# Performance work log

Measured on AMD Instinct MI355X. Metric: run time of the kernel, lower is better.

Reference implementation:

```python
import jax, jax.numpy as jnp
import numpy as np

N = 100000
E = 1600000
D = 128


def setup_inputs() -> dict:
    key = jax.random.key(0)
    k1, k2, k3 = jax.random.split(key, 3)
    indices = jax.random.randint(k1, (2, E), 0, N, dtype=jnp.int32)
    values = jax.random.uniform(k2, (E,), dtype=jnp.float32)
    b = jax.random.normal(k3, (N, D), dtype=jnp.float32)
    return {"values": values, "b": b, "indices": indices, "n": N}


def reference(values, b, indices, n):
    # out = sparse_coo(indices, values, (n, n)) @ b
    # out[i] = sum_{e: row_e == i} values[e] * b[col_e]
    row, col = indices[0], indices[1]
    return jax.ops.segment_sum(values[:, None] * b[col], row, num_segments=n)
```

## Files before the change

### kernel.cpp

```cpp
#include <hip/hip_runtime.h>


#define D_DIM    128
#define RPB      64
#define COLBITS  17
#define COLMASK  ((1 << COLBITS) - 1)
#define NCMAX    512
#define NBMAX    1600
#define CAP      2048
#define NXCD     8

__device__ __forceinline__ unsigned bfr_rne(float f) {
    unsigned u = __float_as_uint(f);
    return (u + 0x7fffu + ((u >> 16) & 1u)) >> 16;
}
__device__ __forceinline__ float bf_lo(unsigned u) { return __uint_as_float(u << 16); }
__device__ __forceinline__ float bf_hi(unsigned u) { return __uint_as_float(u & 0xffff0000u); }

__device__ __forceinline__ int xcd_remap(int bid, int n) {
    int q = n / NXCD, r = n % NXCD;
    int xcd = bid % NXCD, slot = bid / NXCD;
    int base = (xcd < r) ? xcd * (q + 1) : r * (q + 1) + (xcd - r) * q;
    return base + slot;
}

__global__ __launch_bounds__(1024) void k01_fused(
    const int* __restrict__ idx, const float4* __restrict__ b4,
    uint4* __restrict__ bb4, unsigned short* __restrict__ cnt16,
    int E, int NBUX, int CH, int n8) {
    __shared__ int hist[NBMAX];
    int tid = threadIdx.x, c = blockIdx.x;
    int base = c * CH;
    int cnt  = min(CH, E - base);
    for (int i = tid; i < NBUX; i += 1024) hist[i] = 0;
    __syncthreads();
    for (int i = tid; i < cnt; i += 1024)
        atomicAdd(&hist[idx[base + i] >> 6], 1);
    __syncthreads();
    for (int i = tid; i < NBUX; i += 1024)
        cnt16[(size_t)c * NBUX + i] = (unsigned short)hist[i];

    int gstride = gridDim.x * 1024;
    for (int i = blockIdx.x * 1024 + tid; i < n8; i += gstride) {
        float4 a = b4[2 * i];
        float4 d = b4[2 * i + 1];
        uint4 o;
        o.x = bfr_rne(a.x) | (bfr_rne(a.y) << 16);
        o.y = bfr_rne(a.z) | (bfr_rne(a.w) << 16);
        o.z = bfr_rne(d.x) | (bfr_rne(d.y) << 16);
        o.w = bfr_rne(d.z) | (bfr_rne(d.w) << 16);
        bb4[i] = o;
    }
}

__global__ __launch_bounds__(256) void k2a_lofs(
    unsigned short* __restrict__ cnt16, int* __restrict__ total,
    int NCHUNK, int NBUX) {
    int k    = blockIdx.x * 4 + (threadIdx.x >> 6);
    int lane = threadIdx.x & 63;
    if (k >= NBUX) return;
    int PC = (NCHUNK + 63) >> 6;
    int c0 = lane * PC;
    int vals[8];
    int sum = 0;
#pragma unroll
    for (int j = 0; j < 8; ++j) {
        int c = c0 + j;
        vals[j] = (j < PC && c < NCHUNK) ? (int)cnt16[(size_t)c * NBUX + k] : 0;
        sum += vals[j];
    }
    int v = sum;
#pragma unroll
    for (int d = 1; d < 64; d <<= 1) {
        int t = __shfl_up(v, d, 64);
        if (lane >= d) v += t;
    }
    int run = v - sum;
#pragma unroll
    for (int j = 0; j < 8; ++j) {
        int c = c0 + j;
        if (j < PC && c < NCHUNK) {
            cnt16[(size_t)c * NBUX + k] = (unsigned short)run;
            run += vals[j];
        }
    }
    if (lane == 63) total[k] = run;
}

__global__ void k2b_scan(const int* __restrict__ total, int* __restrict__ boff, int n) {
    __shared__ int s[256];
    int t = threadIdx.x;
    int loc[8]; int tot = 0;
#pragma unroll
    for (int j = 0; j < 8; ++j) { int i = t * 8 + j; loc[j] = (i < n) ? total[i] : 0; tot += loc[j]; }
    s[t] = tot; __syncthreads();
    for (int ofs = 1; ofs < 256; ofs <<= 1) {
        int v = (t >= ofs) ? s[t - ofs] : 0; __syncthreads();
        s[t] += v; __syncthreads();
    }
    int run = s[t] - tot;
#pragma unroll
    for (int j = 0; j < 8; ++j) { int i = t * 8 + j; if (i < n) boff[i] = run; run += loc[j]; }
    if (t == 255) boff[n] = s[255];
}

__global__ __launch_bounds__(1024) void k3_scatter(
    const int* __restrict__ idx, const float* __restrict__ values,
    const unsigned short* __restrict__ lofs, const int* __restrict__ boff,
    int2* __restrict__ cv, int E, int NBUX, int CH, int NCHUNK) {
    __shared__ int cur[NBMAX];
    int tid = threadIdx.x;
    int c   = xcd_remap(blockIdx.x, NCHUNK);
    int base = c * CH;
    int cnt  = min(CH, E - base);
    for (int i = tid; i < NBUX; i += 1024)
        cur[i] = boff[i] + (int)lofs[(size_t)c * NBUX + i];
    __syncthreads();
    for (int i = tid; i < cnt; i += 1024) {
        int   row = idx[base + i];
        int   col = idx[E + base + i];
        float v   = values[base + i];
        int pos = atomicAdd(&cur[row >> 6], 1);
        cv[pos] = make_int2(((row & (RPB - 1)) << COLBITS) | col, __float_as_int(v));
    }
}

__global__ __launch_bounds__(256, 8) void k4_reg_bf16(
    const unsigned short* __restrict__ bb, const int2* __restrict__ cv,
    const int* __restrict__ boff, float* __restrict__ out, int N) {
    __shared__ int2 sorted[CAP];
    __shared__ int  rcnt[RPB], roff[RPB], rcur[RPB];

    int tid  = threadIdx.x;
    int lane = tid & 15;
    int grp  = tid >> 4;
    int k    = blockIdx.x;
    int s    = boff[k];
    int cnt  = min(boff[k + 1] - s, CAP);

    if (tid < RPB) rcnt[tid] = 0;

    int2 rec[8];
#pragma unroll
    for (int j = 0; j < 8; ++j) {
        int i = tid + j * 256;
        rec[j] = (i < cnt) ? cv[s + i] : make_int2(0, 0);
    }
    __syncthreads();

#pragma unroll
    for (int j = 0; j < 8; ++j) {
        int i = tid + j * 256;
        if (i < cnt) atomicAdd(&rcnt[rec[j].x >> COLBITS], 1);
    }
    __syncthreads();

    if (tid < 64) {
        int cval = rcnt[tid];
        int v = cval;
#pragma unroll
        for (int d = 1; d < 64; d <<= 1) {
            int t = __shfl_up(v, d, 64);
            if (tid >= d) v += t;
        }
        roff[tid] = v - cval;
        rcur[tid] = v - cval;
    }
    __syncthreads();

#pragma unroll
    for (int j = 0; j < 8; ++j) {
        int i = tid + j * 256;
        if (i < cnt) {
            int pos = atomicAdd(&rcur[rec[j].x >> COLBITS], 1);
            sorted[pos] = rec[j];
        }
    }
    __syncthreads();

    float acc[4][8];
#pragma unroll
    for (int r = 0; r < 4; ++r)
#pragma unroll
        for (int j = 0; j < 8; ++j) acc[r][j] = 0.f;

    const unsigned short* bl = bb + (lane << 3);

#pragma unroll
    for (int r = 0; r < 4; ++r) {
        int lr = (grp << 2) | r;
        int i  = roff[lr];
        int re = rcur[lr];
        for (; i + 1 < re; i += 2) {
            int2 p0 = sorted[i];
            int2 p1 = sorted[i + 1];
            float v0 = __int_as_float(p0.y);
            float v1 = __int_as_float(p1.y);
            const uint4 w0 = *reinterpret_cast<const uint4*>(bl + ((size_t)(p0.x & COLMASK) << 7));
            const uint4 w1 = *reinterpret_cast<const uint4*>(bl + ((size_t)(p1.x & COLMASK) << 7));
            acc[r][0] += v0 * bf_lo(w0.x); acc[r][1] += v0 * bf_hi(w0.x);
            acc[r][2] += v0 * bf_lo(w0.y); acc[r][3] += v0 * bf_hi(w0.y);
            acc[r][4] += v0 * bf_lo(w0.z); acc[r][5] += v0 * bf_hi(w0.z);
            acc[r][6] += v0 * bf_lo(w0.w); acc[r][7] += v0 * bf_hi(w0.w);
            acc[r][0] += v1 * bf_lo(w1.x); acc[r][1] += v1 * bf_hi(w1.x);
            acc[r][2] += v1 * bf_lo(w1.y); acc[r][3] += v1 * bf_hi(w1.y);
            acc[r][4] += v1 * bf_lo(w1.z); acc[r][5] += v1 * bf_hi(w1.z);
            acc[r][6] += v1 * bf_lo(w1.w); acc[r][7] += v1 * bf_hi(w1.w);
        }
        if (i < re) {
            int2 p0 = sorted[i];
            float v0 = __int_as_float(p0.y);
            const uint4 w0 = *reinterpret_cast<const uint4*>(bl + ((size_t)(p0.x & COLMASK) << 7));
            acc[r][0] += v0 * bf_lo(w0.x); acc[r][1] += v0 * bf_hi(w0.x);
            acc[r][2] += v0 * bf_lo(w0.y); acc[r][3] += v0 * bf_hi(w0.y);
            acc[r][4] += v0 * bf_lo(w0.z); acc[r][5] += v0 * bf_hi(w0.z);
            acc[r][6] += v0 * bf_lo(w0.w); acc[r][7] += v0 * bf_hi(w0.w);
        }
    }

#pragma unroll
    for (int r = 0; r < 4; ++r) {
        int row = (k << 6) + (grp << 2) + r;
        if (row < N) {
            float* po = out + ((size_t)row << 7) + (lane << 3);
            *reinterpret_cast<float4*>(po)     = make_float4(acc[r][0], acc[r][1], acc[r][2], acc[r][3]);
            *reinterpret_cast<float4*>(po + 4) = make_float4(acc[r][4], acc[r][5], acc[r][6], acc[r][7]);
        }
    }
}

__global__ __launch_bounds__(256, 8) void k4_sortgather_f32(
    const float* __restrict__ b, const int2* __restrict__ cv,
    const int* __restrict__ boff, float* __restrict__ out, int N) {
    __shared__ int2 sorted[CAP];
    __shared__ int  rcnt[RPB], roff[RPB], rcur[RPB];
    int tid  = threadIdx.x;
    int lane = tid & 31;
    int grp  = tid >> 5;
    int k    = blockIdx.x;
    int s    = boff[k];
    int cnt  = min(boff[k + 1] - s, CAP);
    if (tid < RPB) rcnt[tid] = 0;
    __syncthreads();
    for (int i = tid; i < cnt; i += 256)
        atomicAdd(&rcnt[cv[s + i].x >> COLBITS], 1);
    __syncthreads();
    if (tid < 64) {
        int cval = rcnt[tid];
        int v = cval;
#pragma unroll
        for (int d = 1; d < 64; d <<= 1) {
            int t = __shfl_up(v, d, 64);
            if (tid >= d) v += t;
        }
        roff[tid] = v - cval;
        rcur[tid] = v - cval;
    }
    __syncthreads();
    for (int i = tid; i < cnt; i += 256) {
        int2 p = cv[s + i];
        int pos = atomicAdd(&rcur[p.x >> COLBITS], 1);
        sorted[pos] = p;
    }
    __syncthreads();
    float4 acc[8];
#pragma unroll
    for (int r = 0; r < 8; ++r) acc[r] = make_float4(0.f, 0.f, 0.f, 0.f);
    const float* bl = b + (lane << 2);
#pragma unroll
    for (int r = 0; r < 8; ++r) {
        int lr = (grp << 3) | r;
        int i  = roff[lr];
        int re = rcur[lr];
        for (; i < re; ++i) {
            int2 p0 = sorted[i];
            float v0 = __int_as_float(p0.y);
            const float4 b0 = *reinterpret_cast<const float4*>(bl + (size_t)(p0.x & COLMASK) * D_DIM);
            acc[r].x += v0 * b0.x; acc[r].y += v0 * b0.y;
            acc[r].z += v0 * b0.z; acc[r].w += v0 * b0.w;
        }
    }
#pragma unroll
    for (int r = 0; r < 8; ++r) {
        int row = (k << 6) + (grp << 3) + r;
        if (row < N)
            *reinterpret_cast<float4*>(out + (size_t)row * D_DIM + (lane << 2)) = acc[r];
    }
}

__global__ void spmm_atomic_scatter(const float* __restrict__ values,
                                    const float* __restrict__ b,
                                    const int* __restrict__ indices,
                                    float* __restrict__ out, int E) {
    long long gid = (long long)blockIdx.x * blockDim.x + threadIdx.x;
    long long total = (long long)E * 32;
    if (gid >= total) return;
    int e = (int)(gid >> 5);
    int c = (int)(gid & 31);
    int row = indices[e];
    int col = indices[E + e];
    float v = values[e];
    const float4 bv = *reinterpret_cast<const float4*>(b + (long long)col * D_DIM + (c << 2));
    float* o = out + (long long)row * D_DIM + (c << 2);
    atomicAdd(o + 0, v * bv.x);
    atomicAdd(o + 1, v * bv.y);
    atomicAdd(o + 2, v * bv.z);
    atomicAdd(o + 3, v * bv.w);
}

extern "C" void kernel_launch(void* const* d_in, const int* in_sizes, int n_in,
                              void* d_out, int out_size, void* d_ws, size_t ws_size,
                              hipStream_t stream) {
    const float* values = (const float*)d_in[0];
    const float* b      = (const float*)d_in[1];
    const int*   idx    = (const int*)d_in[2];
    float*       out    = (float*)d_out;

    const int E    = in_sizes[0];
    const int N    = out_size / D_DIM;
    const int NBUX = (N + RPB - 1) / RPB;

    size_t bb_bytes  = ((size_t)N * D_DIM * sizeof(unsigned short) + 15) & ~(size_t)15;
    size_t int_bytes = (((size_t)(NBUX + 1) + NBUX) * sizeof(int) + 15) & ~(size_t)15;
    size_t cv_bytes  = (size_t)E * sizeof(int2);

    int CH = 4096;
    int NCHUNK = (E + CH - 1) / CH;
    size_t c16_bytes = ((size_t)NCHUNK * NBUX * sizeof(unsigned short) + 15) & ~(size_t)15;
    size_t need1 = bb_bytes + int_bytes + c16_bytes + cv_bytes;
    if (ws_size < need1 || NCHUNK > NCMAX) {
        CH = 8192;
        NCHUNK = (E + CH - 1) / CH;
        c16_bytes = ((size_t)NCHUNK * NBUX * sizeof(unsigned short) + 15) & ~(size_t)15;
        need1 = bb_bytes + int_bytes + c16_bytes + cv_bytes;
    }
    size_t need2 = int_bytes + c16_bytes + cv_bytes;

    bool ok_shape = (NBUX <= NBMAX) && (NCHUNK <= NCMAX) && (N <= (1 << COLBITS));
    if (!ok_shape || ws_size < need2) {
        hipMemsetAsync(d_out, 0, (size_t)out_size * sizeof(float), stream);
        long long total = (long long)E * 32;
        int block = 256;
        long long grid = (total + block - 1) / block;
        spmm_atomic_scatter<<<(int)grid, block, 0, stream>>>(values, b, idx, out, E);
        return;
    }

    bool use_bf16 = (ws_size >= need1);
    char* base = (char*)d_ws;
    unsigned short* bb = (unsigned short*)base;
    if (use_bf16) base += bb_bytes;

    int*            boff  = (int*)base;
    int*            total = boff + (NBUX + 1);
    unsigned short* cnt16 = (unsigned short*)(base + int_bytes);
    int2*           cv    = (int2*)(base + int_bytes + c16_bytes);

    int n8 = use_bf16 ? (N * D_DIM) / 8 : 0;
    k01_fused<<<NCHUNK, 1024, 0, stream>>>(idx, (const float4*)b, (uint4*)bb,
                                           cnt16, E, NBUX, CH, n8);
    k2a_lofs<<<(NBUX + 3) / 4, 256, 0, stream>>>(cnt16, total, NCHUNK, NBUX);
    k2b_scan<<<1, 256, 0, stream>>>(total, boff, NBUX);
    k3_scatter<<<NCHUNK, 1024, 0, stream>>>(idx, values, cnt16, boff, cv, E, NBUX, CH, NCHUNK);
    if (use_bf16)
        k4_reg_bf16<<<NBUX, 256, 0, stream>>>(bb, cv, boff, out, N);
    else
        k4_sortgather_f32<<<NBUX, 256, 0, stream>>>(b, cv, boff, out, N);
}
```

Baseline: 107.7 us.

## Vectorize index loads, add nontemporal hints, merge scan kernels via last-block pattern

Row and column indices and values are now read as 4-wide vectors in the histogram and scatter kernels. Streaming loads and stores of b, the packed records and the output use nontemporal hints. The per-bucket scan and the global scan kernel are merged into one launch: the last block to finish, found through an atomic counter, runs the final scan. This removes one launch and cuts load instruction count, at the cost of a threadfence/atomic handshake and an extra alignment guard.

Result: slower. 135.0 us (+25.3%).

```diff
diff --git a/kernel.cpp b/kernel.cpp
--- a/kernel.cpp
+++ b/kernel.cpp
@@ -10,6 +10,10 @@
 #define CAP      2048
 #define NXCD     8
 
+typedef int   i32x4 __attribute__((ext_vector_type(4)));
+typedef float f32x4 __attribute__((ext_vector_type(4)));
+typedef unsigned int u32x4 __attribute__((ext_vector_type(4)));
+
 __device__ __forceinline__ unsigned bfr_rne(float f) {
     unsigned u = __float_as_uint(f);
     return (u + 0x7fffu + ((u >> 16) & 1u)) >> 16;
@@ -25,16 +29,27 @@
 }
 
 __global__ __launch_bounds__(1024) void k01_fused(
-    const int* __restrict__ idx, const float4* __restrict__ b4,
-    uint4* __restrict__ bb4, unsigned short* __restrict__ cnt16,
-    int E, int NBUX, int CH, int n8) {
+    const int* __restrict__ idx, const u32x4* __restrict__ b4,
+    u32x4* __restrict__ bb4, unsigned short* __restrict__ cnt16,
+    int* __restrict__ done, int E, int NBUX, int CH, int n8) {
     __shared__ int hist[NBMAX];
     int tid = threadIdx.x, c = blockIdx.x;
     int base = c * CH;
     int cnt  = min(CH, E - base);
+    if (c == 0 && tid == 0) *done = 0;
     for (int i = tid; i < NBUX; i += 1024) hist[i] = 0;
     __syncthreads();
-    for (int i = tid; i < cnt; i += 1024)
+
+    int nv4 = cnt >> 2;
+    const i32x4* rows4 = (const i32x4*)(idx + base);
+    for (int i = tid; i < nv4; i += 1024) {
+        i32x4 r = rows4[i];
+        atomicAdd(&hist[r.x >> 6], 1);
+        atomicAdd(&hist[r.y >> 6], 1);
+        atomicAdd(&hist[r.z >> 6], 1);
+        atomicAdd(&hist[r.w >> 6], 1);
+    }
+    for (int i = (nv4 << 2) + tid; i < cnt; i += 1024)
         atomicAdd(&hist[idx[base + i] >> 6], 1);
     __syncthreads();
     for (int i = tid; i < NBUX; i += 1024)
@@ -42,72 +57,84 @@
 
     int gstride = gridDim.x * 1024;
     for (int i = blockIdx.x * 1024 + tid; i < n8; i += gstride) {
-        float4 a = b4[2 * i];
-        float4 d = b4[2 * i + 1];
-        uint4 o;
-        o.x = bfr_rne(a.x) | (bfr_rne(a.y) << 16);
-        o.y = bfr_rne(a.z) | (bfr_rne(a.w) << 16);
-        o.z = bfr_rne(d.x) | (bfr_rne(d.y) << 16);
-        o.w = bfr_rne(d.z) | (bfr_rne(d.w) << 16);
+        u32x4 a = __builtin_nontemporal_load(b4 + 2 * i);
+        u32x4 d = __builtin_nontemporal_load(b4 + 2 * i + 1);
+        u32x4 o;
+        o.x = bfr_rne(__uint_as_float(a.x)) | (bfr_rne(__uint_as_float(a.y)) << 16);
+        o.y = bfr_rne(__uint_as_float(a.z)) | (bfr_rne(__uint_as_float(a.w)) << 16);
+        o.z = bfr_rne(__uint_as_float(d.x)) | (bfr_rne(__uint_as_float(d.y)) << 16);
+        o.w = bfr_rne(__uint_as_float(d.z)) | (bfr_rne(__uint_as_float(d.w)) << 16);
         bb4[i] = o;
     }
 }
 
-__global__ __launch_bounds__(256) void k2a_lofs(
+__global__ __launch_bounds__(256) void k2_merged(
     unsigned short* __restrict__ cnt16, int* __restrict__ total,
-    int NCHUNK, int NBUX) {
-    int k    = blockIdx.x * 4 + (threadIdx.x >> 6);
-    int lane = threadIdx.x & 63;
-    if (k >= NBUX) return;
-    int PC = (NCHUNK + 63) >> 6;
-    int c0 = lane * PC;
-    int vals[8];
-    int sum = 0;
-#pragma unroll
-    for (int j = 0; j < 8; ++j) {
-        int c = c0 + j;
-        vals[j] = (j < PC && c < NCHUNK) ? (int)cnt16[(size_t)c * NBUX + k] : 0;
-        sum += vals[j];
-    }
-    int v = sum;
-#pragma unroll
-    for (int d = 1; d < 64; d <<= 1) {
-        int t = __shfl_up(v, d, 64);
-        if (lane >= d) v += t;
-    }
-    int run = v - sum;
-#pragma unroll
-    for (int j = 0; j < 8; ++j) {
-        int c = c0 + j;
-        if (j < PC && c < NCHUNK) {
-            cnt16[(size_t)c * NBUX + k] = (unsigned short)run;
-            run += vals[j];
-        }
-    }
-    if (lane == 63) total[k] = run;
-}
-
-__global__ void k2b_scan(const int* __restrict__ total, int* __restrict__ boff, int n) {
+    int* __restrict__ boff, int* __restrict__ done, int NCHUNK, int NBUX) {
     __shared__ int s[256];
-    int t = threadIdx.x;
+    __shared__ int lastflag;
+    int tid  = threadIdx.x;
+    int k    = blockIdx.x * 4 + (tid >> 6);
+    int lane = tid & 63;
+
+    if (k < NBUX) {
+        int PC = (NCHUNK + 63) >> 6;
+        int c0 = lane * PC;
+        int vals[8];
+        int sum = 0;
+#pragma unroll
+        for (int j = 0; j < 8; ++j) {
+            int c = c0 + j;
+            vals[j] = (j < PC && c < NCHUNK) ? (int)cnt16[(size_t)c * NBUX + k] : 0;
+            sum += vals[j];
+        }
+        int v = sum;
+#pragma unroll
+        for (int d = 1; d < 64; d <<= 1) {
+            int t = __shfl_up(v, d, 64);
+            if (lane >= d) v += t;
+        }
+        int run = v - sum;
+#pragma unroll
+        for (int j = 0; j < 8; ++j) {
+            int c = c0 + j;
+            if (j < PC && c < NCHUNK) {
+                cnt16[(size_t)c * NBUX + k] = (unsigned short)run;
+                run += vals[j];
+            }
+        }
+        if (lane == 63) total[k] = run;
+    }
+    __syncthreads();
+
+    if (tid == 0) {
+        __threadfence();
+        int old = atomicAdd(done, 1);
+        lastflag = (old == (int)gridDim.x - 1);
+    }
+    __syncthreads();
+    if (!lastflag) return;
+    __threadfence();
+
+    int n = NBUX;
     int loc[8]; int tot = 0;
 #pragma unroll
-    for (int j = 0; j < 8; ++j) { int i = t * 8 + j; loc[j] = (i < n) ? total[i] : 0; tot += loc[j]; }
-    s[t] = tot; __syncthreads();
+    for (int j = 0; j < 8; ++j) { int i = tid * 8 + j; loc[j] = (i < n) ? total[i] : 0; tot += loc[j]; }
+    s[tid] = tot; __syncthreads();
     for (int ofs = 1; ofs < 256; ofs <<= 1) {
-        int v = (t >= ofs) ? s[t - ofs] : 0; __syncthreads();
-        s[t] += v; __syncthreads();
-    }
-    int run = s[t] - tot;
-#pragma unroll
-    for (int j = 0; j < 8; ++j) { int i = t * 8 + j; if (i < n) boff[i] = run; run += loc[j]; }
-    if (t == 255) boff[n] = s[255];
+        int v = (tid >= ofs) ? s[tid - ofs] : 0; __syncthreads();
+        s[tid] += v; __syncthreads();
+    }
+    int run2 = s[tid] - tot;
+#pragma unroll
+    for (int j = 0; j < 8; ++j) { int i = tid * 8 + j; if (i < n) boff[i] = run2; run2 += loc[j]; }
+    if (tid == 255) boff[n] = s[255];
 }
 
 __global__ __launch_bounds__(1024) void k3_scatter(
     const int* __restrict__ idx, const float* __restrict__ values,
     const unsigned short* __restrict__ lofs, const int* __restrict__ boff,
-    int2* __restrict__ cv, int E, int NBUX, int CH, int NCHUNK) {
+    int2* __restrict__ cv, int E, int NBUX, int CH, int NCHUNK, int colsAligned) {
     __shared__ int cur[NBMAX];
     int tid = threadIdx.x;
     int c   = xcd_remap(blockIdx.x, NCHUNK);
@@ -116,7 +143,33 @@
     for (int i = tid; i < NBUX; i += 1024)
         cur[i] = boff[i] + (int)lofs[(size_t)c * NBUX + i];
     __syncthreads();
-    for (int i = tid; i < cnt; i += 1024) {
+
+    int nv4 = cnt >> 2;
+    const i32x4* rows4 = (const i32x4*)(idx + base);
+    const f32x4* vals4 = (const f32x4*)(values + base);
+    const i32x4* cols4 = (const i32x4*)(idx + E + base);
+    for (int i = tid; i < nv4; i += 1024) {
+        i32x4 r = rows4[i];
+        f32x4 vv = __builtin_nontemporal_load(vals4 + i);
+        i32x4 cl;
+        if (colsAligned) {
+            cl = __builtin_nontemporal_load(cols4 + i);
+        } else {
+            int e0 = base + (i << 2);
+            cl.x = idx[E + e0]; cl.y = idx[E + e0 + 1];
+            cl.z = idx[E + e0 + 2]; cl.w = idx[E + e0 + 3];
+        }
+        int pos;
+        pos = atomicAdd(&cur[r.x >> 6], 1);
+        cv[pos] = make_int2(((r.x & (RPB - 1)) << COLBITS) | cl.x, __float_as_int(vv.x));
+        pos = atomicAdd(&cur[r.y >> 6], 1);
+        cv[pos] = make_int2(((r.y & (RPB - 1)) << COLBITS) | cl.y, __float_as_int(vv.y));
+        pos = atomicAdd(&cur[r.z >> 6], 1);
+        cv[pos] = make_int2(((r.z & (RPB - 1)) << COLBITS) | cl.z, __float_as_int(vv.z));
+        pos = atomicAdd(&cur[r.w >> 6], 1);
+        cv[pos] = make_int2(((r.w & (RPB - 1)) << COLBITS) | cl.w, __float_as_int(vv.w));
+    }
+    for (int i = (nv4 << 2) + tid; i < cnt; i += 1024) {
         int   row = idx[base + i];
         int   col = idx[E + base + i];
         float v   = values[base + i];
@@ -140,11 +193,18 @@
 
     if (tid < RPB) rcnt[tid] = 0;
 
+    const unsigned long long* cv64 = (const unsigned long long*)cv;
     int2 rec[8];
 #pragma unroll
     for (int j = 0; j < 8; ++j) {
         int i = tid + j * 256;
-        rec[j] = (i < cnt) ? cv[s + i] : make_int2(0, 0);
+        if (i < cnt) {
+            unsigned long long raw = __builtin_nontemporal_load(cv64 + s + i);
+            rec[j].x = (int)(unsigned)(raw & 0xffffffffu);
+            rec[j].y = (int)(unsigned)(raw >> 32);
+        } else {
+            rec[j] = make_int2(0, 0);
+        }
     }
     __syncthreads();
 
@@ -223,8 +283,10 @@
         int row = (k << 6) + (grp << 2) + r;
         if (row < N) {
             float* po = out + ((size_t)row << 7) + (lane << 3);
-            *reinterpret_cast<float4*>(po)     = make_float4(acc[r][0], acc[r][1], acc[r][2], acc[r][3]);
-            *reinterpret_cast<float4*>(po + 4) = make_float4(acc[r][4], acc[r][5], acc[r][6], acc[r][7]);
+            f32x4 o0 = {acc[r][0], acc[r][1], acc[r][2], acc[r][3]};
+            f32x4 o1 = {acc[r][4], acc[r][5], acc[r][6], acc[r][7]};
+            __builtin_nontemporal_store(o0, (f32x4*)po);
+            __builtin_nontemporal_store(o1, (f32x4*)(po + 4));
         }
     }
 }
@@ -321,7 +383,7 @@
     const int NBUX = (N + RPB - 1) / RPB;
 
     size_t bb_bytes  = ((size_t)N * D_DIM * sizeof(unsigned short) + 15) & ~(size_t)15;
-    size_t int_bytes = (((size_t)(NBUX + 1) + NBUX) * sizeof(int) + 15) & ~(size_t)15;
+    size_t int_bytes = (((size_t)(NBUX + 1) + NBUX + 4) * sizeof(int) + 15) & ~(size_t)15;
     size_t cv_bytes  = (size_t)E * sizeof(int2);
 
     int CH = 4096;
@@ -336,7 +398,8 @@
     }
     size_t need2 = int_bytes + c16_bytes + cv_bytes;
 
-    bool ok_shape = (NBUX <= NBMAX) && (NCHUNK <= NCMAX) && (N <= (1 << COLBITS));
+    bool ok_shape = (NBUX <= NBMAX) && (NCHUNK <= NCMAX) && (N <= (1 << COLBITS)) &&
+                    ((CH & 3) == 0);
     if (!ok_shape || ws_size < need2) {
         hipMemsetAsync(d_out, 0, (size_t)out_size * sizeof(float), stream);
         long long total = (long long)E * 32;
@@ -353,15 +416,18 @@
 
     int*            boff  = (int*)base;
     int*            total = boff + (NBUX + 1);
+    int*            done  = total + NBUX;
     unsigned short* cnt16 = (unsigned short*)(base + int_bytes);
     int2*           cv    = (int2*)(base + int_bytes + c16_bytes);
 
     int n8 = use_bf16 ? (N * D_DIM) / 8 : 0;
-    k01_fused<<<NCHUNK, 1024, 0, stream>>>(idx, (const float4*)b, (uint4*)bb,
-                                           cnt16, E, NBUX, CH, n8);
-    k2a_lofs<<<(NBUX + 3) / 4, 256, 0, stream>>>(cnt16, total, NCHUNK, NBUX);
-    k2b_scan<<<1, 256, 0, stream>>>(total, boff, NBUX);
-    k3_scatter<<<NCHUNK, 1024, 0, stream>>>(idx, values, cnt16, boff, cv, E, NBUX, CH, NCHUNK);
+    int colsAligned = ((E & 3) == 0) ? 1 : 0;
+
+    k01_fused<<<NCHUNK, 1024, 0, stream>>>(idx, (const u32x4*)b, (u32x4*)bb,
+                                           cnt16, done, E, NBUX, CH, n8);
+    k2_merged<<<(NBUX + 3) / 4, 256, 0, stream>>>(cnt16, total, boff, done, NCHUNK, NBUX);
+    k3_scatter<<<NCHUNK, 1024, 0, stream>>>(idx, values, cnt16, boff, cv, E, NBUX,
+                                            CH, NCHUNK, colsAligned);
     if (use_bf16)
         k4_reg_bf16<<<NBUX, 256, 0, stream>>>(bb, cv, boff, out, N);
     else
```
